# Kernel tuning notes

Hardware: AMD Instinct MI355X
Metric: run time of the kernel (lower is better)

## Reference

```python
import jax, jax.numpy as jnp
import numpy as np

M0, M1 = 16, 16          # n_modes
C = 64                   # hidden_channels
B = 16                   # batch
H = W = 128              # spatial resolution
SCALE = C ** (-2)        # matches torch: scale * torch.rand(...)


def setup_inputs() -> dict:
    key = jax.random.key(0)
    kx, k0r, k0i, k1r, k1i = jax.random.split(key, 5)
    X = jax.random.normal(kx, (B, C, H, W), dtype=jnp.float32)
    wshape = (C, C, M0, M1)
    # torch.rand with cfloat draws U[0,1) for real and imag parts independently
    w0r = SCALE * jax.random.uniform(k0r, wshape, dtype=jnp.float32)
    w0i = SCALE * jax.random.uniform(k0i, wshape, dtype=jnp.float32)
    w1r = SCALE * jax.random.uniform(k1r, wshape, dtype=jnp.float32)
    w1i = SCALE * jax.random.uniform(k1i, wshape, dtype=jnp.float32)
    return {"X": X, "w0r": w0r, "w0i": w0i, "w1r": w1r, "w1i": w1i}


def reference(X, w0r, w0i, w1r, w1i):
    w0 = w0r + 1j * w0i                       # linear0: (C, C, M0, M1) complex
    w1 = w1r + 1j * w1i                       # linear1
    Xf = jnp.fft.rfftn(X, axes=(-2, -1), norm="forward")   # (B, C, H, W//2+1) complex
    # out[b,c] = sum_t weight[c,t] * Xf[b,t] on the two kept-mode corners
    top = jnp.einsum("ctxy,btxy->bcxy", w0, Xf[:, :, :M0, :M1])
    bot = jnp.einsum("ctxy,btxy->bcxy", w1, Xf[:, :, -M0:, :M1])
    Y = jnp.zeros_like(Xf)
    Y = Y.at[:, :, :M0, :M1].set(top)
    Y = Y.at[:, :, -M0:, :M1].set(bot)
    out = jnp.fft.irfftn(Y, axes=(-2, -1), s=(H, W), norm="forward")
    return out.astype(jnp.float32)
```

## Files before the change

### kernel.cpp

```cpp
#include <hip/hip_runtime.h>

#define PI2 6.28318530717958647692f

__global__ __launch_bounds__(256, 4) void k_fwd(const float* __restrict__ X,
                                                float* __restrict__ Xf) {
  __shared__ __attribute__((aligned(16))) float A2t[17 * 134 * 2];
  __shared__ __attribute__((aligned(16))) float Xc[2][16 * 128];
  const int plane = blockIdx.x;
  const int tid = threadIdx.x;
  const float* Xp = X + (size_t)plane * (128 * 128);

  {
    const int w2 = tid & 63;
    const int kxq = tid >> 6;
    const int r0 = tid >> 5;
    const int col = (tid & 31) * 4;

    float Wr[4], Wi[4], Tr[4], Ti[4];
    #pragma unroll
    for (int j = 0; j < 4; ++j) {
      int s = kxq * 4 + j;
      int kx = (s == 0) ? 16 : s;
      __sincosf(-PI2 * (float)kx / 128.f, &Wi[j], &Wr[j]);
      Tr[j] = 1.f; Ti[j] = 0.f;
    }
    float ar[4][2], ai[4][2];
    #pragma unroll
    for (int j = 0; j < 4; ++j) {
      ar[j][0] = 0.f; ar[j][1] = 0.f; ai[j][0] = 0.f; ai[j][1] = 0.f;
    }
    float dc0 = 0.f, dc1 = 0.f;

    {
      float4 vt = *(const float4*)&Xp[r0 * 128 + col];
      float4 vb = *(const float4*)&Xp[(r0 + 64) * 128 + col];
      *(float4*)&Xc[0][r0 * 128 + col] = vt;
      *(float4*)&Xc[0][(r0 + 8) * 128 + col] = vb;
    }
    __syncthreads();

    for (int c = 0; c < 8; ++c) {
      float4 nt, nb;
      if (c < 7) {
        nt = *(const float4*)&Xp[(8 * (c + 1) + r0) * 128 + col];
        nb = *(const float4*)&Xp[(8 * (c + 1) + r0 + 64) * 128 + col];
      }
      const float* Xb = &Xc[c & 1][0];
      #pragma unroll
      for (int jj = 0; jj < 8; ++jj) {
        float2 tt = *(const float2*)&Xb[jj * 128 + 2 * w2];
        float2 bb = *(const float2*)&Xb[(jj + 8) * 128 + 2 * w2];
        float uex = tt.x + bb.x, uox = tt.x - bb.x;
        float uey = tt.y + bb.y, uoy = tt.y - bb.y;
        ar[0][0] = fmaf(uex, Tr[0], ar[0][0]); ai[0][0] = fmaf(uex, Ti[0], ai[0][0]);
        ar[0][1] = fmaf(uey, Tr[0], ar[0][1]); ai[0][1] = fmaf(uey, Ti[0], ai[0][1]);
        ar[1][0] = fmaf(uox, Tr[1], ar[1][0]); ai[1][0] = fmaf(uox, Ti[1], ai[1][0]);
        ar[1][1] = fmaf(uoy, Tr[1], ar[1][1]); ai[1][1] = fmaf(uoy, Ti[1], ai[1][1]);
        ar[2][0] = fmaf(uex, Tr[2], ar[2][0]); ai[2][0] = fmaf(uex, Ti[2], ai[2][0]);
        ar[2][1] = fmaf(uey, Tr[2], ar[2][1]); ai[2][1] = fmaf(uey, Ti[2], ai[2][1]);
        ar[3][0] = fmaf(uox, Tr[3], ar[3][0]); ai[3][0] = fmaf(uox, Ti[3], ai[3][0]);
        ar[3][1] = fmaf(uoy, Tr[3], ar[3][1]); ai[3][1] = fmaf(uoy, Ti[3], ai[3][1]);
        if (kxq == 0) { dc0 += uex; dc1 += uey; }
        #pragma unroll
        for (int j = 0; j < 4; ++j) {
          float nr = Tr[j] * Wr[j] - Ti[j] * Wi[j];
          float ni = Tr[j] * Wi[j] + Ti[j] * Wr[j];
          Tr[j] = nr; Ti[j] = ni;
        }
      }
      if (c == 3) {
        Tr[0] = 1.f;  Ti[0] = 0.f;
        Tr[1] = 0.f;  Ti[1] = -1.f;
        Tr[2] = -1.f; Ti[2] = 0.f;
        Tr[3] = 0.f;  Ti[3] = 1.f;
      }
      if (c < 7) {
        *(float4*)&Xc[(c + 1) & 1][r0 * 128 + col] = nt;
        *(float4*)&Xc[(c + 1) & 1][(r0 + 8) * 128 + col] = nb;
      }
      __syncthreads();
    }

    #pragma unroll
    for (int j = 0; j < 4; ++j) {
      int s = kxq * 4 + j;
      int row = (s == 0) ? 16 : s;
      *(float4*)&A2t[(row * 134 + 2 * w2) * 2] =
          make_float4(ar[j][0], ai[j][0], ar[j][1], ai[j][1]);
    }
    if (kxq == 0) {
      *(float4*)&A2t[(2 * w2) * 2] = make_float4(dc0, 0.f, dc1, 0.f);
    }
  }
  __syncthreads();

  {
    const int kxi = tid >> 3;
    const int t = tid & 7;
    const int row = (kxi < 16) ? kxi : (32 - kxi);
    const float csign = (kxi < 16) ? 1.f : -1.f;
    const float s = (t & 1) ? -1.f : 1.f;
    float s0r, s0i, s1r, s1i;
    __sincosf(-PI2 * (float)t / 128.f, &s0i, &s0r);
    __sincosf(-PI2 * (float)(t + 8) / 128.f, &s1i, &s1r);
    float r0 = 0.f, i0 = 0.f, r1 = 0.f, i1 = 0.f;
    float E0r = 1.f, E0i = 0.f, E1r = 1.f, E1i = 0.f;
    #pragma unroll
    for (int half = 0; half < 2; ++half) {
      if (half == 1) {
        float c_, s_;
        __sincosf(-1.57079632679489662f * (float)t, &s_, &c_);
        E0r = c_; E0i = s_; E1r = c_; E1i = s_;
      }
      for (int w = half * 32; w < half * 32 + 32; ++w) {
        float2 a = *(const float2*)&A2t[(row * 134 + w) * 2];
        float2 b = *(const float2*)&A2t[(row * 134 + w + 64) * 2];
        float ur = fmaf(s, b.x, a.x);
        float ui = csign * fmaf(s, b.y, a.y);
        r0 = fmaf(ur, E0r, r0); r0 = fmaf(-ui, E0i, r0);
        i0 = fmaf(ur, E0i, i0); i0 = fmaf(ui, E0r, i0);
        r1 = fmaf(ur, E1r, r1); r1 = fmaf(-ui, E1i, r1);
        i1 = fmaf(ur, E1i, i1); i1 = fmaf(ui, E1r, i1);
        float u0 = E0r * s0r - E0i * s0i; E0i = E0r * s0i + E0i * s0r; E0r = u0;
        float u1 = E1r * s1r - E1i * s1i; E1i = E1r * s1i + E1i * s1r; E1r = u1;
      }
    }
    const float sc = 1.f / 16384.f;
    float* base = Xf + (size_t)plane * 1024 + kxi * 32;
    *(float2*)&base[t * 2]       = make_float2(r0 * sc, i0 * sc);
    *(float2*)&base[(t + 8) * 2] = make_float2(r1 * sc, i1 * sc);
  }
}

__global__ __launch_bounds__(256, 2) void k_mix(const float* __restrict__ Xf,
                                                const float* __restrict__ w0r,
                                                const float* __restrict__ w0i,
                                                const float* __restrict__ w1r,
                                                const float* __restrict__ w1i,
                                                float* __restrict__ Y) {
  __shared__ __attribute__((aligned(16))) float Wl[4 * 32 * 16 * 4];
  const int bid = blockIdx.x;
  const int c2 = bid >> 8;
  const int x  = (bid >> 4) & 15;
  const int cg = bid & 15;
  const int c0 = cg * 4;
  const int kxi = c2 * 16 + x;
  const float* Wr_g = c2 ? w1r : w0r;
  const float* Wi_g = c2 ? w1i : w0i;
  const int tid = threadIdx.x;
  const int b = tid >> 4;
  const int y = tid & 15;

  #pragma unroll
  for (int k = 0; k < 16; ++k) {
    int idx = tid + k * 256;
    int y_ = idx & 15, t_ = (idx >> 4) & 63, c_ = idx >> 10;
    size_t ga = (((size_t)(c0 + c_) * 64 + t_) * 16 + x) * 16 + y_;
    int f2i = ((c_ * 32 + (t_ >> 1)) * 16 + y_) * 2 + (t_ & 1);
    *(float2*)&Wl[f2i * 2] = make_float2(Wr_g[ga], Wi_g[ga]);
  }
  __syncthreads();

  float aR[4] = {}, aI[4] = {};
  const float* xbase = Xf + ((size_t)b * 64) * 1024 + kxi * 32 + y * 2;
  for (int t8 = 0; t8 < 64; t8 += 8) {
    float2 xv[8];
    #pragma unroll
    for (int q = 0; q < 8; ++q)
      xv[q] = *(const float2*)&xbase[(size_t)(t8 + q) * 1024];
    #pragma unroll
    for (int p = 0; p < 4; ++p) {
      int t2 = (t8 >> 1) + p;
      float2 xe = xv[2 * p], xo = xv[2 * p + 1];
      #pragma unroll
      for (int cj = 0; cj < 4; ++cj) {
        float4 wv = *(const float4*)&Wl[((cj * 32 + t2) * 16 + y) * 4];
        aR[cj] = fmaf(xe.x, wv.x, aR[cj]); aR[cj] = fmaf(-xe.y, wv.y, aR[cj]);
        aI[cj] = fmaf(xe.x, wv.y, aI[cj]); aI[cj] = fmaf(xe.y, wv.x, aI[cj]);
        aR[cj] = fmaf(xo.x, wv.z, aR[cj]); aR[cj] = fmaf(-xo.y, wv.w, aR[cj]);
        aI[cj] = fmaf(xo.x, wv.w, aI[cj]); aI[cj] = fmaf(xo.y, wv.z, aI[cj]);
      }
    }
  }
  #pragma unroll
  for (int cj = 0; cj < 4; ++cj) {
    size_t ya = ((size_t)(b * 64 + c0 + cj)) * 1024 + kxi * 32 + y * 2;
    *(float2*)&Y[ya] = make_float2(aR[cj], aI[cj]);
  }
}

__global__ __launch_bounds__(256, 4) void k_inv(const float* __restrict__ Y,
                                                float* __restrict__ out) {
  __shared__ __attribute__((aligned(16))) float Yl[1024];
  __shared__ __attribute__((aligned(16))) float Mt[128 * 16 * 2];
  const int plane = blockIdx.x;
  const int tid = threadIdx.x;
  *(float4*)&Yl[tid * 4] = *(const float4*)&Y[(size_t)plane * 1024 + tid * 4];
  __syncthreads();

  {
    const int g = tid >> 6;
    const int h2 = tid & 63;
    float zr[2][4] = {}, zi[2][4] = {};
    float uw, uwi;
    __sincosf(PI2 * (float)h2 / 128.f, &uwi, &uw);
    const float4* Yl4 = (const float4*)Yl;
    float Tr = 1.f, Ti = 0.f;
    #pragma unroll 2
    for (int kxi = 0; kxi < 16; ++kxi) {
      float sgn = (kxi & 1) ? -1.f : 1.f;
      #pragma unroll
      for (int q = 0; q < 2; ++q) {
        float4 p = Yl4[kxi * 8 + g * 2 + q];
        float cr0 = p.x * Tr - p.y * Ti, ci0 = p.x * Ti + p.y * Tr;
        float cr1 = p.z * Tr - p.w * Ti, ci1 = p.z * Ti + p.w * Tr;
        zr[0][2*q]   += cr0; zi[0][2*q]   += ci0;
        zr[0][2*q+1] += cr1; zi[0][2*q+1] += ci1;
        zr[1][2*q]   = fmaf(sgn, cr0, zr[1][2*q]);   zi[1][2*q]   = fmaf(sgn, ci0, zi[1][2*q]);
        zr[1][2*q+1] = fmaf(sgn, cr1, zr[1][2*q+1]); zi[1][2*q+1] = fmaf(sgn, ci1, zi[1][2*q+1]);
      }
      float nr = Tr * uw - Ti * uwi, ni = Tr * uwi + Ti * uw;
      Tr = nr; Ti = ni;
    }
    __sincosf(PI2 * (float)((112 * h2) & 127) / 128.f, &Ti, &Tr);
    #pragma unroll 2
    for (int kxi = 16; kxi < 32; ++kxi) {
      float sgn = (kxi & 1) ? -1.f : 1.f;
      #pragma unroll
      for (int q = 0; q < 2; ++q) {
        float4 p = Yl4[kxi * 8 + g * 2 + q];
        float cr0 = p.x * Tr - p.y * Ti, ci0 = p.x * Ti + p.y * Tr;
        float cr1 = p.z * Tr - p.w * Ti, ci1 = p.z * Ti + p.w * Tr;
        zr[0][2*q]   += cr0; zi[0][2*q]   += ci0;
        zr[0][2*q+1] += cr1; zi[0][2*q+1] += ci1;
        zr[1][2*q]   = fmaf(sgn, cr0, zr[1][2*q]);   zi[1][2*q]   = fmaf(sgn, ci0, zi[1][2*q]);
        zr[1][2*q+1] = fmaf(sgn, cr1, zr[1][2*q+1]); zi[1][2*q+1] = fmaf(sgn, ci1, zi[1][2*q+1]);
      }
      float nr = Tr * uw - Ti * uwi, ni = Tr * uwi + Ti * uw;
      Tr = nr; Ti = ni;
    }
    #pragma unroll
    for (int hs = 0; hs < 2; ++hs) {
      int h = h2 + hs * 64;
      #pragma unroll
      for (int q = 0; q < 2; ++q) {
        int ky0 = g * 4 + 2 * q;
        float f0 = (ky0 == 0) ? 1.f : 2.f;
        float4 v = make_float4(f0 * zr[hs][2*q],   -f0 * zi[hs][2*q],
                               2.f * zr[hs][2*q+1], -2.f * zi[hs][2*q+1]);
        int f4i = h * 8 + ((g * 2 + q) ^ (h & 7));
        *(float4*)&Mt[f4i * 4] = v;
      }
    }
  }
  __syncthreads();

  {
    const int hp = tid >> 5;
    const int w2 = tid & 31;
    float C[16], S[16];
    {
      float cw, sw;
      __sincosf(PI2 * (float)w2 / 128.f, &sw, &cw);
      C[0] = 1.f; S[0] = 0.f;
      #pragma unroll
      for (int k = 1; k < 16; ++k) {
        C[k] = C[k - 1] * cw - S[k - 1] * sw;
        S[k] = C[k - 1] * sw + S[k - 1] * cw;
      }
    }
    float* op = out + (size_t)plane * (128 * 128);
    const float4* Mt4 = (const float4*)Mt;
    #pragma unroll 2
    for (int hj = 0; hj < 16; ++hj) {
      int h = hp * 16 + hj;
      float e = 0.f, o = 0.f, e2 = 0.f, o2 = 0.f;
      #pragma unroll
      for (int j = 0; j < 8; ++j) {
        float4 m = Mt4[h * 8 + (j ^ (h & 7))];
        int k0 = 2 * j, k1 = 2 * j + 1;
        e = fmaf(m.x, C[k0], e); e = fmaf(m.y, S[k0], e);
        o = fmaf(m.z, C[k1], o); o = fmaf(m.w, S[k1], o);
        if ((k0 & 2) == 0) { e2 = fmaf(m.x, C[k0], e2); e2 = fmaf(m.y, S[k0], e2); }
        else               { e2 = fmaf(-m.x, C[k0], e2); e2 = fmaf(-m.y, S[k0], e2); }
        if ((k1 & 2) == 0) { o2 = fmaf(m.w, C[k1], o2); o2 = fmaf(-m.z, S[k1], o2); }
        else               { o2 = fmaf(-m.w, C[k1], o2); o2 = fmaf(m.z, S[k1], o2); }
      }
      op[h * 128 + w2]      = e + o;
      op[h * 128 + w2 + 64] = e - o;
      op[h * 128 + w2 + 32] = e2 + o2;
      op[h * 128 + w2 + 96] = e2 - o2;
    }
  }
}

extern "C" void kernel_launch(void* const* d_in, const int* in_sizes, int n_in,
                              void* d_out, int out_size, void* d_ws, size_t ws_size,
                              hipStream_t stream) {
  const float* X   = (const float*)d_in[0];
  const float* w0r = (const float*)d_in[1];
  const float* w0i = (const float*)d_in[2];
  const float* w1r = (const float*)d_in[3];
  const float* w1i = (const float*)d_in[4];
  float* outp = (float*)d_out;
  float* Xf = (float*)d_ws;
  float* Yw = (float*)d_ws + (1u << 20);
  k_fwd<<<1024, 256, 0, stream>>>(X, Xf);
  k_mix<<<512, 256, 0, stream>>>(Xf, w0r, w0i, w1r, w1i, Yw);
  k_inv<<<1024, 256, 0, stream>>>(Yw, outp);
}
```

Baseline: 166.6 us.

## Deepen forward row staging to four-slot smaller chunks and raise unroll factors

```diff
diff --git a/kernel.cpp b/kernel.cpp
--- a/kernel.cpp
+++ b/kernel.cpp
@@ -5,7 +5,7 @@
 __global__ __launch_bounds__(256, 4) void k_fwd(const float* __restrict__ X,
                                                 float* __restrict__ Xf) {
   __shared__ __attribute__((aligned(16))) float A2t[17 * 134 * 2];
-  __shared__ __attribute__((aligned(16))) float Xc[2][16 * 128];
+  __shared__ __attribute__((aligned(16))) float Xc[4][8 * 128];
   const int plane = blockIdx.x;
   const int tid = threadIdx.x;
   const float* Xp = X + (size_t)plane * (128 * 128);
@@ -13,7 +13,7 @@
   {
     const int w2 = tid & 63;
     const int kxq = tid >> 6;
-    const int r0 = tid >> 5;
+    const int lrow = tid >> 5;
     const int col = (tid & 31) * 4;
 
     float Wr[4], Wi[4], Tr[4], Ti[4];
@@ -32,24 +32,31 @@
     float dc0 = 0.f, dc1 = 0.f;
 
     {
-      float4 vt = *(const float4*)&Xp[r0 * 128 + col];
-      float4 vb = *(const float4*)&Xp[(r0 + 64) * 128 + col];
-      *(float4*)&Xc[0][r0 * 128 + col] = vt;
-      *(float4*)&Xc[0][(r0 + 8) * 128 + col] = vb;
+      float4 v0, v1, v2;
+      int r0g = (lrow < 4) ? lrow : (60 + lrow);
+      int r1g = (lrow < 4) ? (4 + lrow) : (64 + lrow);
+      int r2g = (lrow < 4) ? (8 + lrow) : (68 + lrow);
+      v0 = *(const float4*)&Xp[r0g * 128 + col];
+      v1 = *(const float4*)&Xp[r1g * 128 + col];
+      v2 = *(const float4*)&Xp[r2g * 128 + col];
+      *(float4*)&Xc[0][lrow * 128 + col] = v0;
+      *(float4*)&Xc[1][lrow * 128 + col] = v1;
+      *(float4*)&Xc[2][lrow * 128 + col] = v2;
     }
     __syncthreads();
 
-    for (int c = 0; c < 8; ++c) {
-      float4 nt, nb;
-      if (c < 7) {
-        nt = *(const float4*)&Xp[(8 * (c + 1) + r0) * 128 + col];
-        nb = *(const float4*)&Xp[(8 * (c + 1) + r0 + 64) * 128 + col];
-      }
-      const float* Xb = &Xc[c & 1][0];
-      #pragma unroll
-      for (int jj = 0; jj < 8; ++jj) {
+    for (int c = 0; c < 16; ++c) {
+      float4 nv;
+      if (c < 13) {
+        int rg = (lrow < 4) ? (4 * (c + 3) + lrow)
+                            : (60 + 4 * (c + 3) + lrow);
+        nv = *(const float4*)&Xp[rg * 128 + col];
+      }
+      const float* Xb = &Xc[c & 3][0];
+      #pragma unroll
+      for (int jj = 0; jj < 4; ++jj) {
         float2 tt = *(const float2*)&Xb[jj * 128 + 2 * w2];
-        float2 bb = *(const float2*)&Xb[(jj + 8) * 128 + 2 * w2];
+        float2 bb = *(const float2*)&Xb[(jj + 4) * 128 + 2 * w2];
         float uex = tt.x + bb.x, uox = tt.x - bb.x;
         float uey = tt.y + bb.y, uoy = tt.y - bb.y;
         ar[0][0] = fmaf(uex, Tr[0], ar[0][0]); ai[0][0] = fmaf(uex, Ti[0], ai[0][0]);
@@ -68,16 +75,14 @@
           Tr[j] = nr; Ti[j] = ni;
         }
       }
-      if (c == 3) {
+      if (c == 7) {
         Tr[0] = 1.f;  Ti[0] = 0.f;
         Tr[1] = 0.f;  Ti[1] = -1.f;
         Tr[2] = -1.f; Ti[2] = 0.f;
         Tr[3] = 0.f;  Ti[3] = 1.f;
       }
-      if (c < 7) {
-        *(float4*)&Xc[(c + 1) & 1][r0 * 128 + col] = nt;
-        *(float4*)&Xc[(c + 1) & 1][(r0 + 8) * 128 + col] = nb;
-      }
+      if (c < 13)
+        *(float4*)&Xc[(c + 3) & 3][lrow * 128 + col] = nv;
       __syncthreads();
     }
 
@@ -112,6 +117,7 @@
         __sincosf(-1.57079632679489662f * (float)t, &s_, &c_);
         E0r = c_; E0i = s_; E1r = c_; E1i = s_;
       }
+      #pragma unroll 4
       for (int w = half * 32; w < half * 32 + 32; ++w) {
         float2 a = *(const float2*)&A2t[(row * 134 + w) * 2];
         float2 b = *(const float2*)&A2t[(row * 134 + w + 64) * 2];
@@ -206,7 +212,7 @@
     __sincosf(PI2 * (float)h2 / 128.f, &uwi, &uw);
     const float4* Yl4 = (const float4*)Yl;
     float Tr = 1.f, Ti = 0.f;
-    #pragma unroll 2
+    #pragma unroll 4
     for (int kxi = 0; kxi < 16; ++kxi) {
       float sgn = (kxi & 1) ? -1.f : 1.f;
       #pragma unroll
@@ -223,7 +229,7 @@
       Tr = nr; Ti = ni;
     }
     __sincosf(PI2 * (float)((112 * h2) & 127) / 128.f, &Ti, &Tr);
-    #pragma unroll 2
+    #pragma unroll 4
     for (int kxi = 16; kxi < 32; ++kxi) {
       float sgn = (kxi & 1) ? -1.f : 1.f;
       #pragma unroll
@@ -271,7 +277,7 @@
     }
     float* op = out + (size_t)plane * (128 * 128);
     const float4* Mt4 = (const float4*)Mt;
-    #pragma unroll 2
+    #pragma unroll 4
     for (int hj = 0; hj < 16; ++hj) {
       int h = hp * 16 + hj;
       float e = 0.f, o = 0.f, e2 = 0.f, o2 = 0.f;
```

Result: no change. 169.6 us (+1.8%).
